# Performance work log

Hardware: AMD Instinct MI355X
Metric: run time of the kernel (lower is better)

Reference implementation:

```python
import jax, jax.numpy as jnp
import numpy as np

L, H, NH, NKV, HD, FF, V = 2, 2048, 16, 2, 128, 11008, 32000
B, S, R, LORA_SCALE = 32, 64, 16, 2.0  # lora scaling = alpha/r = 32/16
PH, TD = 1024, 512
ROPE_THETA = 1e6

def _rms(x, w, eps=1e-6):
    return x * jax.lax.rsqrt(jnp.mean(x * x, axis=-1, keepdims=True) + eps) * w

def _rot_half(x):
    h = x.shape[-1] // 2
    return jnp.concatenate([-x[..., h:], x[..., :h]], axis=-1)

def _lora_linear(x, W, A, Bm, b=None):
    y = x @ W.T + LORA_SCALE * ((x @ A.T) @ Bm.T)
    return y + b if b is not None else y

def _forward(input_ids, attention_mask, embed, Wq, bq, Aq, Bq, Wk, bk, Ak, Bk,
             Wv, bv, Av, Bv, Wo, Ao, Bo, ln1, ln2, Wg, Wu, Wd, norm_f,
             W1, b1, W2, b2):
    Bsz, Sl = input_ids.shape
    h = embed[input_ids]                                            # [B,S,H]
    inv_freq = 1.0 / (ROPE_THETA ** (jnp.arange(0, HD, 2, dtype=jnp.float32) / HD))
    ang = jnp.arange(Sl, dtype=jnp.float32)[:, None] * inv_freq      # [S,HD/2]
    cos = jnp.concatenate([jnp.cos(ang)] * 2, -1)[None, :, None, :]  # [1,S,1,HD]
    sin = jnp.concatenate([jnp.sin(ang)] * 2, -1)[None, :, None, :]
    causal = jnp.tril(jnp.ones((Sl, Sl), dtype=bool))
    keep = causal[None, None] & (attention_mask[:, None, None, :] > 0)
    bias = jnp.where(keep, 0.0, -1e9).astype(jnp.float32)            # [B,1,S,S]
    for l in range(L):
        x = _rms(h, ln1[l])
        q = _lora_linear(x, Wq[l], Aq[l], Bq[l], bq[l]).reshape(Bsz, Sl, NH, HD)
        k = _lora_linear(x, Wk[l], Ak[l], Bk[l], bk[l]).reshape(Bsz, Sl, NKV, HD)
        v = _lora_linear(x, Wv[l], Av[l], Bv[l], bv[l]).reshape(Bsz, Sl, NKV, HD)
        q = q * cos + _rot_half(q) * sin
        k = k * cos + _rot_half(k) * sin
        k = jnp.repeat(k, NH // NKV, axis=2)                         # GQA expand
        v = jnp.repeat(v, NH // NKV, axis=2)
        scores = jnp.einsum('bqhd,bkhd->bhqk', q, k) / np.sqrt(HD).astype(np.float32) + bias
        p = jax.nn.softmax(scores, axis=-1)
        attn = jnp.einsum('bhqk,bkhd->bqhd', p, v).reshape(Bsz, Sl, H)
        h = h + _lora_linear(attn, Wo[l], Ao[l], Bo[l])
        x = _rms(h, ln2[l])
        h = h + (jax.nn.silu(x @ Wg[l].T) * (x @ Wu[l].T)) @ Wd[l].T  # SwiGLU MLP
    h = _rms(h, norm_f)                       # final norm -> hidden_states[-1]
    seq_len = jnp.sum(attention_mask, axis=1) - 1
    pooled = h[jnp.arange(Bsz), seq_len]      # last valid token  [B,H]
    z = jax.nn.gelu(pooled @ W1.T + b1, approximate=False)
    return (z @ W2.T + b2).astype(jnp.float32)  # [B,512]

def setup_inputs():
    key = jax.random.key(0)
    ks = jax.random.split(key, 32)
    def n(k, shape, s=0.02):
        return (s * jax.random.normal(k, shape)).astype(jnp.float32)
    lens = jax.random.randint(ks[0], (B,), 1, S + 1)
    return {
        'input_ids': jax.random.randint(ks[1], (B, S), 0, V, dtype=jnp.int32),
        'attention_mask': (jnp.arange(S)[None, :] < lens[:, None]).astype(jnp.int32),
        'embed': n(ks[2], (V, H)),
        'Wq': n(ks[3], (L, H, H)), 'bq': n(ks[4], (L, H)),
        'Aq': n(ks[5], (L, R, H)), 'Bq': n(ks[6], (L, H, R)),
        'Wk': n(ks[7], (L, NKV * HD, H)), 'bk': n(ks[8], (L, NKV * HD)),
        'Ak': n(ks[9], (L, R, H)), 'Bk': n(ks[10], (L, NKV * HD, R)),
        'Wv': n(ks[11], (L, NKV * HD, H)), 'bv': n(ks[12], (L, NKV * HD)),
        'Av': n(ks[13], (L, R, H)), 'Bv': n(ks[14], (L, NKV * HD, R)),
        'Wo': n(ks[15], (L, H, H)),
        'Ao': n(ks[16], (L, R, H)), 'Bo': n(ks[17], (L, H, R)),
        'ln1': jnp.ones((L, H), jnp.float32), 'ln2': jnp.ones((L, H), jnp.float32),
        'Wg': n(ks[18], (L, FF, H)), 'Wu': n(ks[19], (L, FF, H)), 'Wd': n(ks[20], (L, H, FF)),
        'norm_f': jnp.ones((H,), jnp.float32),
        'W1': n(ks[21], (PH, H)), 'b1': jnp.zeros((PH,), jnp.float32),
        'W2': n(ks[22], (TD, PH)), 'b2': jnp.zeros((TD,), jnp.float32),
    }

def reference(input_ids, attention_mask, embed, Wq, bq, Aq, Bq, Wk, bk, Ak, Bk,
              Wv, bv, Av, Bv, Wo, Ao, Bo, ln1, ln2, Wg, Wu, Wd, norm_f,
              W1, b1, W2, b2):
    return _forward(input_ids, attention_mask, embed, Wq, bq, Aq, Bq, Wk, bk, Ak, Bk,
                    Wv, bv, Av, Bv, Wo, Ao, Bo, ln1, ln2, Wg, Wu, Wd, norm_f,
                    W1, b1, W2, b2)
```

## Files before the change

kernel.cpp:

```cpp
#include <hip/hip_runtime.h>
#include <hip/hip_bf16.h>
#include <math.h>

namespace {
constexpr int NL  = 2;
constexpr int H   = 2048;
constexpr int NH  = 16;
constexpr int NKV = 2;
constexpr int HD  = 128;
constexpr int FF  = 11008;
constexpr int BB  = 32;
constexpr int SS  = 64;
constexpr int RR  = 16;
constexpr int TT  = BB * SS;
constexpr int KVD = NKV * HD;
constexpr int QKVD = H + 2 * KVD;
constexpr int PH  = 1024, TDm = 512;
constexpr float LSCALE = 2.0f;
}

typedef __bf16 bf16x8 __attribute__((ext_vector_type(8)));
typedef float  f32x4  __attribute__((ext_vector_type(4)));

__device__ __forceinline__ ushort4 f4_to_bf4(float4 r) {
  __hip_bfloat16 a = __float2bfloat16(r.x), b = __float2bfloat16(r.y),
                 c = __float2bfloat16(r.z), d = __float2bfloat16(r.w);
  return make_ushort4(*(unsigned short*)&a, *(unsigned short*)&b,
                      *(unsigned short*)&c, *(unsigned short*)&d);
}

__global__ __launch_bounds__(256) void k_embed(const int* __restrict__ ids,
                                               const float* __restrict__ emb,
                                               float* __restrict__ h) {
  int t = blockIdx.x;
  long id = ids[t];
  const float4* src = reinterpret_cast<const float4*>(emb + id * (long)H);
  float4* dst = reinterpret_cast<float4*>(h + (long)t * H);
  for (int i = threadIdx.x; i < H / 4; i += 256) dst[i] = src[i];
}

__global__ __launch_bounds__(256) void k_cvt(const float* __restrict__ src,
                                             __hip_bfloat16* __restrict__ dst, long n) {
  long i = ((long)blockIdx.x * 256 + threadIdx.x) * 4;
  if (i >= n) return;
  float4 v = *reinterpret_cast<const float4*>(src + i);
  *reinterpret_cast<ushort4*>(dst + i) = f4_to_bf4(v);
}

__global__ __launch_bounds__(256) void k_rmsnorm(const float* __restrict__ in,
                                                 const float* __restrict__ w,
                                                 float* __restrict__ out,
                                                 __hip_bfloat16* __restrict__ outb) {
  int t = blockIdx.x, tid = threadIdx.x;
  const float4* xr = reinterpret_cast<const float4*>(in + (long)t * H);
  float4 v0 = xr[tid], v1 = xr[tid + 256];
  float ss = v0.x*v0.x + v0.y*v0.y + v0.z*v0.z + v0.w*v0.w
           + v1.x*v1.x + v1.y*v1.y + v1.z*v1.z + v1.w*v1.w;
  #pragma unroll
  for (int off = 32; off; off >>= 1) ss += __shfl_xor(ss, off);
  __shared__ float sred[4];
  if ((tid & 63) == 0) sred[tid >> 6] = ss;
  __syncthreads();
  float scale = rsqrtf((sred[0] + sred[1] + sred[2] + sred[3]) * (1.0f / H) + 1e-6f);
  const float4* wr = reinterpret_cast<const float4*>(w);
  float4 w0 = wr[tid], w1 = wr[tid + 256];
  float4 r0 = make_float4(v0.x*scale*w0.x, v0.y*scale*w0.y, v0.z*scale*w0.z, v0.w*scale*w0.w);
  float4 r1 = make_float4(v1.x*scale*w1.x, v1.y*scale*w1.y, v1.z*scale*w1.z, v1.w*scale*w1.w);
  float4* o = reinterpret_cast<float4*>(out + (long)t * H);
  o[tid] = r0; o[tid + 256] = r1;
  ushort4* ob = reinterpret_cast<ushort4*>(outb + (long)t * H);
  ob[tid] = f4_to_bf4(r0); ob[tid + 256] = f4_to_bf4(r1);
}

enum { ME_BIAS_F32 = 0, ME_ACC_F32 = 1, ME_SILU_BF16 = 2, ME_MUL_BF16 = 3 };

__device__ __forceinline__ int raster_sw(int bid, int nwg) {
  int q8 = nwg >> 3, r8 = nwg & 7;
  int xcd = bid & 7, pos = bid >> 3;
  return (xcd < r8 ? xcd * (q8 + 1) : r8 * (q8 + 1) + (xcd - r8) * q8) + pos;
}

template <int EPI, int BM, int BN, int WROWS, int WCOLS>
__global__ __launch_bounds__(256) void k_mgemm(
    const __hip_bfloat16* __restrict__ Abf,
    const __hip_bfloat16* __restrict__ Wbf,
    const float* __restrict__ bias,
    float* __restrict__ Cf,
    __hip_bfloat16* Cb,
    const __hip_bfloat16* gate,
    int M, int N, int K) {
  constexpr int BK = 32;
  constexpr int WTM = BM / WROWS, WTN = BN / WCOLS;
  constexpr int FM = WTM / 16, FN = WTN / 16;
  constexpr int ACH = BM * BK / 8, BCH = BN * BK / 8;
  __shared__ __align__(16) __bf16 As[2][BM * BK];
  __shared__ __align__(16) __bf16 Bs[2][BN * BK];
  const int tid = threadIdx.x;
  const int sw = raster_sw(blockIdx.x, gridDim.x);
  const int ntm = M / BM;
  const int bm = (sw % ntm) * BM, bn = (sw / ntm) * BN;
  const int lane = tid & 63, wv = tid >> 6;
  const int wm = (wv / WCOLS) * WTM, wn = (wv % WCOLS) * WTN;
  const int lr15 = lane & 15;
  const int lks = (((lane >> 4) << 3)) ^ ((((lr15 >> 1) & 3)) << 3);
  f32x4 acc[FM][FN] = {};
  const __bf16* Ag = reinterpret_cast<const __bf16*>(Abf) + (long)bm * K;
  const __bf16* Bg = reinterpret_cast<const __bf16*>(Wbf) + (long)bn * K;

  auto stage = [&](int buf, int k0) {
    #pragma unroll
    for (int i = tid; i < ACH; i += 256)
      __builtin_amdgcn_global_load_lds(
          (const __attribute__((address_space(1))) void*)
            (Ag + (long)(i >> 2) * K + k0 + (((i & 3) ^ ((i >> 3) & 3)) << 3)),
          (__attribute__((address_space(3))) void*)(&As[buf][i * 8]), 16, 0, 0);
    #pragma unroll
    for (int i = tid; i < BCH; i += 256)
      __builtin_amdgcn_global_load_lds(
          (const __attribute__((address_space(1))) void*)
            (Bg + (long)(i >> 2) * K + k0 + (((i & 3) ^ ((i >> 3) & 3)) << 3)),
          (__attribute__((address_space(3))) void*)(&Bs[buf][i * 8]), 16, 0, 0);
  };
  auto compute = [&](int buf) {
    bf16x8 af[FM], bfr[FN];
    #pragma unroll
    for (int m = 0; m < FM; ++m)
      af[m] = *reinterpret_cast<const bf16x8*>(&As[buf][(wm + m * 16 + lr15) * BK + lks]);
    #pragma unroll
    for (int n = 0; n < FN; ++n)
      bfr[n] = *reinterpret_cast<const bf16x8*>(&Bs[buf][(wn + n * 16 + lr15) * BK + lks]);
    #pragma unroll
    for (int m = 0; m < FM; ++m)
      #pragma unroll
      for (int n = 0; n < FN; ++n)
        acc[m][n] = __builtin_amdgcn_mfma_f32_16x16x32_bf16(af[m], bfr[n], acc[m][n], 0, 0, 0);
  };

  stage(0, 0);
  asm volatile("s_waitcnt vmcnt(0)" ::: "memory");
  __builtin_amdgcn_s_barrier();
  int cur = 0;
  for (int k0 = BK; k0 < K; k0 += BK) {
    stage(cur ^ 1, k0);
    compute(cur);
    asm volatile("s_waitcnt vmcnt(0)" ::: "memory");
    __builtin_amdgcn_s_barrier();
    cur ^= 1;
  }
  compute(cur);

  const int r0 = (lane >> 4) << 2;
  #pragma unroll
  for (int m = 0; m < FM; ++m)
    #pragma unroll
    for (int n = 0; n < FN; ++n) {
      const int col = bn + wn + n * 16 + lr15;
      const long rowb = bm + wm + m * 16 + r0;
      #pragma unroll
      for (int j = 0; j < 4; ++j) {
        const long off = (rowb + j) * N + col;
        float v = acc[m][n][j];
        if constexpr (EPI == ME_BIAS_F32) {
          Cf[off] = v + bias[col];
        } else if constexpr (EPI == ME_ACC_F32) {
          Cf[off] += v;
        } else if constexpr (EPI == ME_SILU_BF16) {
          Cb[off] = __float2bfloat16(v / (1.0f + expf(-v)));
        } else {
          float g = __bfloat162float(gate[off]);
          Cb[off] = __float2bfloat16(v * g);
        }
      }
    }
}

template <int BM, int BN, int WROWS, int WCOLS>
__global__ __launch_bounds__(256, 2) void k_swiglu(
    const __hip_bfloat16* __restrict__ Abf,
    const __hip_bfloat16* __restrict__ Wgb,
    const __hip_bfloat16* __restrict__ Wub,
    __hip_bfloat16* __restrict__ Cb,
    int M, int N, int K) {
  constexpr int BK = 32;
  constexpr int WTM = BM / WROWS, WTN = BN / WCOLS;
  constexpr int FM = WTM / 16, FN = WTN / 16;
  constexpr int ACH = BM * BK / 8, BCH = BN * BK / 8;
  __shared__ __align__(16) __bf16 As[2][BM * BK];
  __shared__ __align__(16) __bf16 Gs[2][BN * BK];
  __shared__ __align__(16) __bf16 Us[2][BN * BK];
  const int tid = threadIdx.x;
  const int sw = raster_sw(blockIdx.x, gridDim.x);
  const int ntm = M / BM;
  const int bm = (sw % ntm) * BM, bn = (sw / ntm) * BN;
  const int lane = tid & 63, wv = tid >> 6;
  const int wm = (wv / WCOLS) * WTM, wn = (wv % WCOLS) * WTN;
  const int lr15 = lane & 15;
  const int lks = (((lane >> 4) << 3)) ^ ((((lr15 >> 1) & 3)) << 3);
  f32x4 accg[FM][FN] = {}, accu[FM][FN] = {};
  const __bf16* Ag = reinterpret_cast<const __bf16*>(Abf) + (long)bm * K;
  const __bf16* Gg = reinterpret_cast<const __bf16*>(Wgb) + (long)bn * K;
  const __bf16* Ug = reinterpret_cast<const __bf16*>(Wub) + (long)bn * K;

  auto stage = [&](int buf, int k0) {
    #pragma unroll
    for (int i = tid; i < ACH; i += 256)
      __builtin_amdgcn_global_load_lds(
          (const __attribute__((address_space(1))) void*)
            (Ag + (long)(i >> 2) * K + k0 + (((i & 3) ^ ((i >> 3) & 3)) << 3)),
          (__attribute__((address_space(3))) void*)(&As[buf][i * 8]), 16, 0, 0);
    #pragma unroll
    for (int i = tid; i < BCH; i += 256)
      __builtin_amdgcn_global_load_lds(
          (const __attribute__((address_space(1))) void*)
            (Gg + (long)(i >> 2) * K + k0 + (((i & 3) ^ ((i >> 3) & 3)) << 3)),
          (__attribute__((address_space(3))) void*)(&Gs[buf][i * 8]), 16, 0, 0);
    #pragma unroll
    for (int i = tid; i < BCH; i += 256)
      __builtin_amdgcn_global_load_lds(
          (const __attribute__((address_space(1))) void*)
            (Ug + (long)(i >> 2) * K + k0 + (((i & 3) ^ ((i >> 3) & 3)) << 3)),
          (__attribute__((address_space(3))) void*)(&Us[buf][i * 8]), 16, 0, 0);
  };
  auto compute = [&](int buf) {
    bf16x8 af[FM], gf[FN], uf[FN];
    #pragma unroll
    for (int m = 0; m < FM; ++m)
      af[m] = *reinterpret_cast<const bf16x8*>(&As[buf][(wm + m * 16 + lr15) * BK + lks]);
    #pragma unroll
    for (int n = 0; n < FN; ++n) {
      gf[n] = *reinterpret_cast<const bf16x8*>(&Gs[buf][(wn + n * 16 + lr15) * BK + lks]);
      uf[n] = *reinterpret_cast<const bf16x8*>(&Us[buf][(wn + n * 16 + lr15) * BK + lks]);
    }
    #pragma unroll
    for (int m = 0; m < FM; ++m)
      #pragma unroll
      for (int n = 0; n < FN; ++n) {
        accg[m][n] = __builtin_amdgcn_mfma_f32_16x16x32_bf16(af[m], gf[n], accg[m][n], 0, 0, 0);
        accu[m][n] = __builtin_amdgcn_mfma_f32_16x16x32_bf16(af[m], uf[n], accu[m][n], 0, 0, 0);
      }
  };

  stage(0, 0);
  asm volatile("s_waitcnt vmcnt(0)" ::: "memory");
  __builtin_amdgcn_s_barrier();
  int cur = 0;
  for (int k0 = BK; k0 < K; k0 += BK) {
    stage(cur ^ 1, k0);
    compute(cur);
    asm volatile("s_waitcnt vmcnt(0)" ::: "memory");
    __builtin_amdgcn_s_barrier();
    cur ^= 1;
  }
  compute(cur);

  const int r0 = (lane >> 4) << 2;
  #pragma unroll
  for (int m = 0; m < FM; ++m)
    #pragma unroll
    for (int n = 0; n < FN; ++n) {
      const int col = bn + wn + n * 16 + lr15;
      const long rowb = bm + wm + m * 16 + r0;
      #pragma unroll
      for (int j = 0; j < 4; ++j) {
        float g = accg[m][n][j], u = accu[m][n][j];
        Cb[(rowb + j) * N + col] = __float2bfloat16((g / (1.0f + expf(-g))) * u);
      }
    }
}

enum { EPI_STORE = 0, EPI_GELU = 3 };

template <int EPI, bool HAS_BIAS>
__global__ __launch_bounds__(256) void k_gemm(const float* __restrict__ A,
                                              const float* __restrict__ W,
                                              const float* __restrict__ bias,
                                              float* __restrict__ C,
                                              int M, int N, int K) {
  constexpr int BM = 64, BN = 64, BK = 16;
  __shared__ float As[BK][BM + 4];
  __shared__ float Ws[BK][BN + 4];
  const int bm = blockIdx.y * BM, bn = blockIdx.x * BN;
  const int tid = threadIdx.x;
  const int lr = tid >> 2;
  const int lc = (tid & 3) << 2;
  const int ty = tid >> 4, tx = tid & 15;
  float acc[4][4] = {};
  const int arow = bm + lr;
  const bool aok = arow < M;
  const float* Ap = A + (long)arow * K + lc;
  const float* Wp = W + (long)(bn + lr) * K + lc;
  for (int k0 = 0; k0 < K; k0 += BK) {
    float4 av = aok ? *reinterpret_cast<const float4*>(Ap + k0) : make_float4(0.f, 0.f, 0.f, 0.f);
    float4 wv = *reinterpret_cast<const float4*>(Wp + k0);
    As[lc + 0][lr] = av.x; As[lc + 1][lr] = av.y; As[lc + 2][lr] = av.z; As[lc + 3][lr] = av.w;
    Ws[lc + 0][lr] = wv.x; Ws[lc + 1][lr] = wv.y; Ws[lc + 2][lr] = wv.z; Ws[lc + 3][lr] = wv.w;
    __syncthreads();
    #pragma unroll
    for (int k = 0; k < BK; ++k) {
      float4 a4 = *reinterpret_cast<const float4*>(&As[k][ty << 2]);
      float4 b4 = *reinterpret_cast<const float4*>(&Ws[k][tx << 2]);
      float a[4] = {a4.x, a4.y, a4.z, a4.w};
      float b[4] = {b4.x, b4.y, b4.z, b4.w};
      #pragma unroll
      for (int i = 0; i < 4; ++i)
        #pragma unroll
        for (int j = 0; j < 4; ++j) acc[i][j] = fmaf(a[i], b[j], acc[i][j]);
    }
    __syncthreads();
  }
  const int col = bn + (tx << 2);
  #pragma unroll
  for (int i = 0; i < 4; ++i) {
    int row = bm + (ty << 2) + i;
    if (row < M) {
      float4 r = make_float4(acc[i][0], acc[i][1], acc[i][2], acc[i][3]);
      if (HAS_BIAS) {
        float4 bv = *reinterpret_cast<const float4*>(bias + col);
        r.x += bv.x; r.y += bv.y; r.z += bv.z; r.w += bv.w;
      }
      if (EPI == EPI_GELU) {
        r.x = 0.5f * r.x * (1.0f + erff(r.x * 0.70710678118654752f));
        r.y = 0.5f * r.y * (1.0f + erff(r.y * 0.70710678118654752f));
        r.z = 0.5f * r.z * (1.0f + erff(r.z * 0.70710678118654752f));
        r.w = 0.5f * r.w * (1.0f + erff(r.w * 0.70710678118654752f));
      }
      *reinterpret_cast<float4*>(C + (long)row * N + col) = r;
    }
  }
}

__global__ __launch_bounds__(256) void k_lora_down(const float* __restrict__ x,
                                                   const float* __restrict__ A,
                                                   float* __restrict__ tmp) {
  int t = blockIdx.x, tid = threadIdx.x;
  int r = tid & 15, sl = tid >> 4;
  const float* xr = x + (long)t * H + sl * 128;
  const float* Ar = A + (long)r * H + sl * 128;
  float p = 0.f;
  #pragma unroll 8
  for (int kk = 0; kk < 128; kk += 4) {
    float4 xv = *reinterpret_cast<const float4*>(xr + kk);
    float4 av = *reinterpret_cast<const float4*>(Ar + kk);
    p = fmaf(xv.x, av.x, p); p = fmaf(xv.y, av.y, p);
    p = fmaf(xv.z, av.z, p); p = fmaf(xv.w, av.w, p);
  }
  __shared__ float red[16][17];
  red[sl][r] = p;
  __syncthreads();
  if (tid < 16) {
    float s = 0.f;
    #pragma unroll
    for (int i = 0; i < 16; ++i) s += red[i][tid];
    tmp[t * RR + tid] = s;
  }
}

__global__ __launch_bounds__(256) void k_lora_add(const float* __restrict__ tmp,
                                                  const float* __restrict__ Bm,
                                                  float* __restrict__ C, int ldC, int N) {
  long idx = (long)blockIdx.x * 256 + threadIdx.x;
  if (idx >= (long)TT * N) return;
  int t = (int)(idx / N), n = (int)(idx % N);
  const float* tr = tmp + (long)t * RR;
  const float* br = Bm + (long)n * RR;
  float s = 0.f;
  #pragma unroll
  for (int r = 0; r < RR; ++r) s = fmaf(tr[r], br[r], s);
  C[(long)t * ldC + n] += LSCALE * s;
}

__global__ __launch_bounds__(256) void k_rope(float* __restrict__ qkv) {
  int t = blockIdx.x;
  float pos = (float)(t & (SS - 1));
  float* row = qkv + (long)t * QKVD;
  for (int idx = threadIdx.x; idx < NH * 64 + NKV * 64; idx += 256) {
    float* base;
    int j;
    if (idx < NH * 64) {
      int head = idx >> 6; j = idx & 63;
      base = row + head * HD;
    } else {
      int i2 = idx - NH * 64;
      int head = i2 >> 6; j = i2 & 63;
      base = row + H + head * HD;
    }
    float inv = 1.0f / powf(1.0e6f, (float)(2 * j) * (1.0f / HD));
    float ang = pos * inv;
    float cs = cosf(ang), sn = sinf(ang);
    float lo = base[j], hi = base[j + 64];
    base[j]      = lo * cs - hi * sn;
    base[j + 64] = hi * cs + lo * sn;
  }
}

__global__ __launch_bounds__(64) void k_attn(const float* __restrict__ qkv,
                                             const int* __restrict__ mask,
                                             float* __restrict__ o,
                                             __hip_bfloat16* __restrict__ obf) {
  int flat = blockIdx.x;
  int qi = flat & (SS - 1);
  int hh = (flat >> 6) & (NH - 1);
  int b  = flat >> 10;
  int lane = threadIdx.x;
  int kv = hh >> 3;
  long t = (long)b * SS + qi;
  const float* qr = qkv + t * QKVD + hh * HD;
  const float* kr = qkv + ((long)b * SS + lane) * QKVD + H + kv * HD;
  float dot = 0.f;
  #pragma unroll 8
  for (int d = 0; d < HD; d += 4) {
    float4 qv = *reinterpret_cast<const float4*>(qr + d);
    float4 kvv = *reinterpret_cast<const float4*>(kr + d);
    dot = fmaf(qv.x, kvv.x, dot); dot = fmaf(qv.y, kvv.y, dot);
    dot = fmaf(qv.z, kvv.z, dot); dot = fmaf(qv.w, kvv.w, dot);
  }
  bool keep = (lane <= qi) && (mask[b * SS + lane] > 0);
  float sc = dot * 0.08838834764831845f + (keep ? 0.f : -1e9f);
  float m = sc;
  #pragma unroll
  for (int off = 32; off; off >>= 1) m = fmaxf(m, __shfl_xor(m, off));
  float e = expf(sc - m);
  float s = e;
  #pragma unroll
  for (int off = 32; off; off >>= 1) s += __shfl_xor(s, off);
  float p = e / s;
  __shared__ float pl[64];
  pl[lane] = p;
  __syncthreads();
  float o0 = 0.f, o1 = 0.f;
  const float* vb = qkv + (long)b * SS * QKVD + H + KVD + kv * HD;
  for (int ki = 0; ki < SS; ++ki) {
    float pp = pl[ki];
    o0 = fmaf(pp, vb[(long)ki * QKVD + lane], o0);
    o1 = fmaf(pp, vb[(long)ki * QKVD + lane + 64], o1);
  }
  long oidx = t * H + hh * HD + lane;
  o[oidx] = o0;
  o[oidx + 64] = o1;
  __hip_bfloat16 b0 = __float2bfloat16(o0), b1 = __float2bfloat16(o1);
  obf[oidx] = b0;
  obf[oidx + 64] = b1;
}

__global__ __launch_bounds__(256) void k_pool(const float* __restrict__ x,
                                              const int* __restrict__ mask,
                                              float* __restrict__ pooled) {
  int b = blockIdx.x;
  __shared__ int len;
  if (threadIdx.x == 0) {
    int L2 = 0;
    for (int i = 0; i < SS; ++i) L2 += (mask[b * SS + i] > 0);
    len = L2;
  }
  __syncthreads();
  const float4* sp = reinterpret_cast<const float4*>(x + ((long)b * SS + len - 1) * H);
  float4* dp = reinterpret_cast<float4*>(pooled + (long)b * H);
  for (int i = threadIdx.x; i < H / 4; i += 256) dp[i] = sp[i];
}

static inline int cvt_grid(long n) { return (int)((n / 4 + 255) / 256); }

extern "C" void kernel_launch(void* const* d_in, const int* in_sizes, int n_in,
                              void* d_out, int out_size, void* d_ws, size_t ws_size,
                              hipStream_t stream) {
  const int*   ids    = (const int*)d_in[0];
  const int*   mask   = (const int*)d_in[1];
  const float* embed  = (const float*)d_in[2];
  const float* Wq     = (const float*)d_in[3];
  const float* bq     = (const float*)d_in[4];
  const float* Aq     = (const float*)d_in[5];
  const float* Bq     = (const float*)d_in[6];
  const float* Wk     = (const float*)d_in[7];
  const float* bk     = (const float*)d_in[8];
  const float* Ak     = (const float*)d_in[9];
  const float* Bk     = (const float*)d_in[10];
  const float* Wv     = (const float*)d_in[11];
  const float* bv     = (const float*)d_in[12];
  const float* Av     = (const float*)d_in[13];
  const float* Bv     = (const float*)d_in[14];
  const float* Wo     = (const float*)d_in[15];
  const float* Ao     = (const float*)d_in[16];
  const float* Bo     = (const float*)d_in[17];
  const float* ln1    = (const float*)d_in[18];
  const float* ln2    = (const float*)d_in[19];
  const float* Wg     = (const float*)d_in[20];
  const float* Wu     = (const float*)d_in[21];
  const float* Wd     = (const float*)d_in[22];
  const float* norm_f = (const float*)d_in[23];
  const float* W1     = (const float*)d_in[24];
  const float* b1     = (const float*)d_in[25];
  const float* W2     = (const float*)d_in[26];
  const float* b2     = (const float*)d_in[27];

  float* ws = (float*)d_ws;
  float* h       = ws;
  float* x       = h    + (long)TT * H;
  float* qkv     = x    + (long)TT * H;
  float* tmpR    = qkv  + (long)TT * QKVD;
  float* pooled  = tmpR + (long)TT * RR;
  float* zz      = pooled + (long)BB * H;
  float* biascat = zz   + (long)BB * PH;
  float* endf32  = biascat + QKVD;
  __hip_bfloat16* x_bf = (__hip_bfloat16*)endf32;
  __hip_bfloat16* ffbf = x_bf + (long)TT * H;
  __hip_bfloat16* wbf  = ffbf + (long)TT * FF;
  __hip_bfloat16* wbf2 = wbf  + (long)FF * H;
  size_t need_fused = (size_t)((char*)(wbf2 + (long)FF * H) - (char*)d_ws);
  bool fused_ok = ws_size >= need_fused;

  k_embed<<<TT, 256, 0, stream>>>(ids, embed, h);

  for (int l = 0; l < NL; ++l) {
    const long lHH = (long)l * H * H;
    const long lKH = (long)l * KVD * H;
    const long lRH = (long)l * RR * H;
    k_rmsnorm<<<TT, 256, 0, stream>>>(h, ln1 + l * H, x, x_bf);
    k_cvt<<<cvt_grid((long)H * H), 256, 0, stream>>>(Wq + lHH, wbf, (long)H * H);
    k_cvt<<<cvt_grid((long)KVD * H), 256, 0, stream>>>(Wk + lKH, wbf + (long)H * H, (long)KVD * H);
    k_cvt<<<cvt_grid((long)KVD * H), 256, 0, stream>>>(Wv + lKH, wbf + (long)(H + KVD) * H, (long)KVD * H);
    hipMemcpyAsync(biascat,           bq + (long)l * H,   H * sizeof(float),   hipMemcpyDeviceToDevice, stream);
    hipMemcpyAsync(biascat + H,       bk + (long)l * KVD, KVD * sizeof(float), hipMemcpyDeviceToDevice, stream);
    hipMemcpyAsync(biascat + H + KVD, bv + (long)l * KVD, KVD * sizeof(float), hipMemcpyDeviceToDevice, stream);
    k_mgemm<ME_BIAS_F32, 128, 128, 2, 2><<<(TT / 128) * (QKVD / 128), 256, 0, stream>>>(
        x_bf, wbf, biascat, qkv, nullptr, nullptr, TT, QKVD, H);
    k_lora_down<<<TT, 256, 0, stream>>>(x, Aq + lRH, tmpR);
    k_lora_add<<<((long)TT * H + 255) / 256, 256, 0, stream>>>(tmpR, Bq + (long)l * H * RR, qkv, QKVD, H);
    k_lora_down<<<TT, 256, 0, stream>>>(x, Ak + lRH, tmpR);
    k_lora_add<<<((long)TT * KVD + 255) / 256, 256, 0, stream>>>(tmpR, Bk + (long)l * KVD * RR, qkv + H, QKVD, KVD);
    k_lora_down<<<TT, 256, 0, stream>>>(x, Av + lRH, tmpR);
    k_lora_add<<<((long)TT * KVD + 255) / 256, 256, 0, stream>>>(tmpR, Bv + (long)l * KVD * RR, qkv + H + KVD, QKVD, KVD);
    k_rope<<<TT, 256, 0, stream>>>(qkv);
    k_attn<<<BB * NH * SS, 64, 0, stream>>>(qkv, mask, x, x_bf);
    k_lora_down<<<TT, 256, 0, stream>>>(x, Ao + lRH, tmpR);
    k_cvt<<<cvt_grid((long)H * H), 256, 0, stream>>>(Wo + lHH, wbf, (long)H * H);
    k_mgemm<ME_ACC_F32, 64, 128, 2, 2><<<(TT / 64) * (H / 128), 256, 0, stream>>>(
        x_bf, wbf, nullptr, h, nullptr, nullptr, TT, H, H);
    k_lora_add<<<((long)TT * H + 255) / 256, 256, 0, stream>>>(tmpR, Bo + (long)l * H * RR, h, H, H);
    k_rmsnorm<<<TT, 256, 0, stream>>>(h, ln2 + l * H, x, x_bf);
    if (fused_ok) {
      k_cvt<<<cvt_grid((long)FF * H), 256, 0, stream>>>(Wg + (long)l * FF * H, wbf, (long)FF * H);
      k_cvt<<<cvt_grid((long)FF * H), 256, 0, stream>>>(Wu + (long)l * FF * H, wbf2, (long)FF * H);
      k_swiglu<128, 128, 2, 2><<<(TT / 128) * (FF / 128), 256, 0, stream>>>(
          x_bf, wbf, wbf2, ffbf, TT, FF, H);
    } else {
      k_cvt<<<cvt_grid((long)FF * H), 256, 0, stream>>>(Wg + (long)l * FF * H, wbf, (long)FF * H);
      k_mgemm<ME_SILU_BF16, 128, 128, 2, 2><<<(TT / 128) * (FF / 128), 256, 0, stream>>>(
          x_bf, wbf, nullptr, nullptr, ffbf, nullptr, TT, FF, H);
      k_cvt<<<cvt_grid((long)FF * H), 256, 0, stream>>>(Wu + (long)l * FF * H, wbf, (long)FF * H);
      k_mgemm<ME_MUL_BF16, 128, 128, 2, 2><<<(TT / 128) * (FF / 128), 256, 0, stream>>>(
          x_bf, wbf, nullptr, nullptr, ffbf, ffbf, TT, FF, H);
    }
    k_cvt<<<cvt_grid((long)H * FF), 256, 0, stream>>>(Wd + (long)l * H * FF, wbf, (long)H * FF);
    k_mgemm<ME_ACC_F32, 64, 128, 2, 2><<<(TT / 64) * (H / 128), 256, 0, stream>>>(
        ffbf, wbf, nullptr, h, nullptr, nullptr, TT, H, FF);
  }

  k_rmsnorm<<<TT, 256, 0, stream>>>(h, norm_f, x, x_bf);
  k_pool<<<BB, 256, 0, stream>>>(x, mask, pooled);
  k_gemm<EPI_GELU, true><<<dim3(PH / 64, 1), 256, 0, stream>>>(pooled, W1, b1, zz, BB, PH, H);
  k_gemm<EPI_STORE, true><<<dim3(TDm / 64, 1), 256, 0, stream>>>(zz, W2, b2, (float*)d_out, BB, TDm, PH);
}
```

Measured before the change: 2.146 ms.

## Triple-buffer GEMM LDS staging with partial vmcnt waits; enlarge Wo/Wd tiles

The MFMA GEMM and fused SwiGLU kernels go from double to triple buffering. Two k-slabs are prefetched ahead, and a partial s_waitcnt vmcnt waits only for the oldest stage's loads, so global-to-LDS loads overlap more compute. The Wo and Wd projection GEMMs also switch from 64x128 to 128x128 tiles, raising reuse but halving the grid to 256 blocks. Triple buffering raises LDS use per block, which may lower occupancy, especially for the SwiGLU kernel with three operand buffers.

```diff
diff --git a/kernel.cpp b/kernel.cpp
--- a/kernel.cpp
+++ b/kernel.cpp
@@ -29,6 +29,16 @@
                       *(unsigned short*)&c, *(unsigned short*)&d);
 }
 
+template <int N> __device__ __forceinline__ void wait_vm() {
+  static_assert(N == 0 || N == 3 || N == 4 || N == 6 || N == 8 || N == 12, "add case");
+  if constexpr (N == 0)      asm volatile("s_waitcnt vmcnt(0)" ::: "memory");
+  else if constexpr (N == 3) asm volatile("s_waitcnt vmcnt(3)" ::: "memory");
+  else if constexpr (N == 4) asm volatile("s_waitcnt vmcnt(4)" ::: "memory");
+  else if constexpr (N == 6) asm volatile("s_waitcnt vmcnt(6)" ::: "memory");
+  else if constexpr (N == 8) asm volatile("s_waitcnt vmcnt(8)" ::: "memory");
+  else                       asm volatile("s_waitcnt vmcnt(12)" ::: "memory");
+}
+
 __global__ __launch_bounds__(256) void k_embed(const int* __restrict__ ids,
                                                const float* __restrict__ emb,
                                                float* __restrict__ h) {
@@ -93,8 +103,9 @@
   constexpr int WTM = BM / WROWS, WTN = BN / WCOLS;
   constexpr int FM = WTM / 16, FN = WTN / 16;
   constexpr int ACH = BM * BK / 8, BCH = BN * BK / 8;
-  __shared__ __align__(16) __bf16 As[2][BM * BK];
-  __shared__ __align__(16) __bf16 Bs[2][BN * BK];
+  constexpr int LPT = (ACH + BCH) / 256;
+  __shared__ __align__(16) __bf16 As[3][BM * BK];
+  __shared__ __align__(16) __bf16 Bs[3][BN * BK];
   const int tid = threadIdx.x;
   const int sw = raster_sw(blockIdx.x, gridDim.x);
   const int ntm = M / BM;
@@ -136,18 +147,20 @@
         acc[m][n] = __builtin_amdgcn_mfma_f32_16x16x32_bf16(af[m], bfr[n], acc[m][n], 0, 0, 0);
   };
 
+  const int NS = K / BK;
   stage(0, 0);
-  asm volatile("s_waitcnt vmcnt(0)" ::: "memory");
+  stage(1, BK);
+  wait_vm<LPT>();
   __builtin_amdgcn_s_barrier();
-  int cur = 0;
-  for (int k0 = BK; k0 < K; k0 += BK) {
-    stage(cur ^ 1, k0);
-    compute(cur);
-    asm volatile("s_waitcnt vmcnt(0)" ::: "memory");
-    __builtin_amdgcn_s_barrier();
-    cur ^= 1;
-  }
-  compute(cur);
+  for (int t = 0; t < NS; ++t) {
+    if (t + 2 < NS) stage((t + 2) % 3, (t + 2) * BK);
+    compute(t % 3);
+    if (t + 1 < NS) {
+      if (t + 2 < NS) wait_vm<LPT>();
+      else            wait_vm<0>();
+      __builtin_amdgcn_s_barrier();
+    }
+  }
 
   const int r0 = (lane >> 4) << 2;
   #pragma unroll
@@ -185,9 +198,10 @@
   constexpr int WTM = BM / WROWS, WTN = BN / WCOLS;
   constexpr int FM = WTM / 16, FN = WTN / 16;
   constexpr int ACH = BM * BK / 8, BCH = BN * BK / 8;
-  __shared__ __align__(16) __bf16 As[2][BM * BK];
-  __shared__ __align__(16) __bf16 Gs[2][BN * BK];
-  __shared__ __align__(16) __bf16 Us[2][BN * BK];
+  constexpr int LPT = (ACH + 2 * BCH) / 256;
+  __shared__ __align__(16) __bf16 As[3][BM * BK];
+  __shared__ __align__(16) __bf16 Gs[3][BN * BK];
+  __shared__ __align__(16) __bf16 Us[3][BN * BK];
   const int tid = threadIdx.x;
   const int sw = raster_sw(blockIdx.x, gridDim.x);
   const int ntm = M / BM;
@@ -240,18 +254,20 @@
       }
   };
 
+  const int NS = K / BK;
   stage(0, 0);
-  asm volatile("s_waitcnt vmcnt(0)" ::: "memory");
+  stage(1, BK);
+  wait_vm<LPT>();
   __builtin_amdgcn_s_barrier();
-  int cur = 0;
-  for (int k0 = BK; k0 < K; k0 += BK) {
-    stage(cur ^ 1, k0);
-    compute(cur);
-    asm volatile("s_waitcnt vmcnt(0)" ::: "memory");
-    __builtin_amdgcn_s_barrier();
-    cur ^= 1;
-  }
-  compute(cur);
+  for (int t = 0; t < NS; ++t) {
+    if (t + 2 < NS) stage((t + 2) % 3, (t + 2) * BK);
+    compute(t % 3);
+    if (t + 1 < NS) {
+      if (t + 2 < NS) wait_vm<LPT>();
+      else            wait_vm<0>();
+      __builtin_amdgcn_s_barrier();
+    }
+  }
 
   const int r0 = (lane >> 4) << 2;
   #pragma unroll
@@ -533,7 +549,7 @@
     k_attn<<<BB * NH * SS, 64, 0, stream>>>(qkv, mask, x, x_bf);
     k_lora_down<<<TT, 256, 0, stream>>>(x, Ao + lRH, tmpR);
     k_cvt<<<cvt_grid((long)H * H), 256, 0, stream>>>(Wo + lHH, wbf, (long)H * H);
-    k_mgemm<ME_ACC_F32, 64, 128, 2, 2><<<(TT / 64) * (H / 128), 256, 0, stream>>>(
+    k_mgemm<ME_ACC_F32, 128, 128, 2, 2><<<(TT / 128) * (H / 128), 256, 0, stream>>>(
         x_bf, wbf, nullptr, h, nullptr, nullptr, TT, H, H);
     k_lora_add<<<((long)TT * H + 255) / 256, 256, 0, stream>>>(tmpR, Bo + (long)l * H * RR, h, H, H);
     k_rmsnorm<<<TT, 256, 0, stream>>>(h, ln2 + l * H, x, x_bf);
@@ -551,7 +567,7 @@
           x_bf, wbf, nullptr, nullptr, ffbf, ffbf, TT, FF, H);
     }
     k_cvt<<<cvt_grid((long)H * FF), 256, 0, stream>>>(Wd + (long)l * H * FF, wbf, (long)H * FF);
-    k_mgemm<ME_ACC_F32, 64, 128, 2, 2><<<(TT / 64) * (H / 128), 256, 0, stream>>>(
+    k_mgemm<ME_ACC_F32, 128, 128, 2, 2><<<(TT / 128) * (H / 128), 256, 0, stream>>>(
         ffbf, wbf, nullptr, h, nullptr, nullptr, TT, H, FF);
   }
 
```

New measurement: 2.353 ms. +9.6%, slower.

## Use 512-thread 128x128 GEMM tiles and precompute RoPE cos/sin table

Applied to the files above, without the earlier changes.

Fixes the mfma GEMM kernel at 128x128 tiles with 8 waves (2x4 warp grid, 64x32 per wave) and 512 threads, including the Wo and down projections that previously used 64x128 tiles. This halves the block count for those two GEMMs and doubles the waves per block, aiming for more reuse per tile and better latency hiding. RoPE cos/sin values are now computed once into a workspace table instead of calling powf/cosf/sinf per element in every layer. Larger tiles on the N=2048 GEMMs leave only 256 blocks, which may underfill the GPU.

```diff
diff --git a/kernel.cpp b/kernel.cpp
--- a/kernel.cpp
+++ b/kernel.cpp
@@ -80,8 +80,8 @@
   return (xcd < r8 ? xcd * (q8 + 1) : r8 * (q8 + 1) + (xcd - r8) * q8) + pos;
 }
 
-template <int EPI, int BM, int BN, int WROWS, int WCOLS>
-__global__ __launch_bounds__(256) void k_mgemm(
+template <int EPI>
+__global__ __launch_bounds__(512) void k_mgemm(
     const __hip_bfloat16* __restrict__ Abf,
     const __hip_bfloat16* __restrict__ Wbf,
     const float* __restrict__ bias,
@@ -89,9 +89,8 @@
     __hip_bfloat16* Cb,
     const __hip_bfloat16* gate,
     int M, int N, int K) {
-  constexpr int BK = 32;
-  constexpr int WTM = BM / WROWS, WTN = BN / WCOLS;
-  constexpr int FM = WTM / 16, FN = WTN / 16;
+  constexpr int BM = 128, BN = 128, BK = 32;
+  constexpr int FM = 4, FN = 2;
   constexpr int ACH = BM * BK / 8, BCH = BN * BK / 8;
   __shared__ __align__(16) __bf16 As[2][BM * BK];
   __shared__ __align__(16) __bf16 Bs[2][BN * BK];
@@ -100,7 +99,7 @@
   const int ntm = M / BM;
   const int bm = (sw % ntm) * BM, bn = (sw / ntm) * BN;
   const int lane = tid & 63, wv = tid >> 6;
-  const int wm = (wv / WCOLS) * WTM, wn = (wv % WCOLS) * WTN;
+  const int wm = (wv >> 2) * 64, wn = (wv & 3) * 32;
   const int lr15 = lane & 15;
   const int lks = (((lane >> 4) << 3)) ^ ((((lr15 >> 1) & 3)) << 3);
   f32x4 acc[FM][FN] = {};
@@ -109,13 +108,13 @@
 
   auto stage = [&](int buf, int k0) {
     #pragma unroll
-    for (int i = tid; i < ACH; i += 256)
+    for (int i = tid; i < ACH; i += 512)
       __builtin_amdgcn_global_load_lds(
           (const __attribute__((address_space(1))) void*)
             (Ag + (long)(i >> 2) * K + k0 + (((i & 3) ^ ((i >> 3) & 3)) << 3)),
           (__attribute__((address_space(3))) void*)(&As[buf][i * 8]), 16, 0, 0);
     #pragma unroll
-    for (int i = tid; i < BCH; i += 256)
+    for (int i = tid; i < BCH; i += 512)
       __builtin_amdgcn_global_load_lds(
           (const __attribute__((address_space(1))) void*)
             (Bg + (long)(i >> 2) * K + k0 + (((i & 3) ^ ((i >> 3) & 3)) << 3)),
@@ -369,9 +368,19 @@
   C[(long)t * ldC + n] += LSCALE * s;
 }
 
-__global__ __launch_bounds__(256) void k_rope(float* __restrict__ qkv) {
+__global__ __launch_bounds__(256) void k_rope_tab(float2* __restrict__ tab) {
+  int idx = blockIdx.x * 256 + threadIdx.x;
+  if (idx >= SS * 64) return;
+  int pos = idx >> 6, j = idx & 63;
+  float inv = 1.0f / powf(1.0e6f, (float)(2 * j) * (1.0f / HD));
+  float ang = (float)pos * inv;
+  tab[idx] = make_float2(cosf(ang), sinf(ang));
+}
+
+__global__ __launch_bounds__(256) void k_rope(float* __restrict__ qkv,
+                                              const float2* __restrict__ tab) {
   int t = blockIdx.x;
-  float pos = (float)(t & (SS - 1));
+  const float2* trow = tab + (t & (SS - 1)) * 64;
   float* row = qkv + (long)t * QKVD;
   for (int idx = threadIdx.x; idx < NH * 64 + NKV * 64; idx += 256) {
     float* base;
@@ -384,12 +393,10 @@
       int head = i2 >> 6; j = i2 & 63;
       base = row + H + head * HD;
     }
-    float inv = 1.0f / powf(1.0e6f, (float)(2 * j) * (1.0f / HD));
-    float ang = pos * inv;
-    float cs = cosf(ang), sn = sinf(ang);
+    float2 cs2 = trow[j];
     float lo = base[j], hi = base[j + 64];
-    base[j]      = lo * cs - hi * sn;
-    base[j + 64] = hi * cs + lo * sn;
+    base[j]      = lo * cs2.x - hi * cs2.y;
+    base[j + 64] = hi * cs2.x + lo * cs2.y;
   }
 }
 
@@ -500,7 +507,8 @@
   float* pooled  = tmpR + (long)TT * RR;
   float* zz      = pooled + (long)BB * H;
   float* biascat = zz   + (long)BB * PH;
-  float* endf32  = biascat + QKVD;
+  float2* ropetab = (float2*)(biascat + QKVD);
+  float* endf32  = (float*)(ropetab + SS * 64);
   __hip_bfloat16* x_bf = (__hip_bfloat16*)endf32;
   __hip_bfloat16* ffbf = x_bf + (long)TT * H;
   __hip_bfloat16* wbf  = ffbf + (long)TT * FF;
@@ -509,6 +517,7 @@
   bool fused_ok = ws_size >= need_fused;
 
   k_embed<<<TT, 256, 0, stream>>>(ids, embed, h);
+  k_rope_tab<<<(SS * 64 + 255) / 256, 256, 0, stream>>>(ropetab);
 
   for (int l = 0; l < NL; ++l) {
     const long lHH = (long)l * H * H;
@@ -521,7 +530,7 @@
     hipMemcpyAsync(biascat,           bq + (long)l * H,   H * sizeof(float),   hipMemcpyDeviceToDevice, stream);
     hipMemcpyAsync(biascat + H,       bk + (long)l * KVD, KVD * sizeof(float), hipMemcpyDeviceToDevice, stream);
     hipMemcpyAsync(biascat + H + KVD, bv + (long)l * KVD, KVD * sizeof(float), hipMemcpyDeviceToDevice, stream);
-    k_mgemm<ME_BIAS_F32, 128, 128, 2, 2><<<(TT / 128) * (QKVD / 128), 256, 0, stream>>>(
+    k_mgemm<ME_BIAS_F32><<<(TT / 128) * (QKVD / 128), 512, 0, stream>>>(
         x_bf, wbf, biascat, qkv, nullptr, nullptr, TT, QKVD, H);
     k_lora_down<<<TT, 256, 0, stream>>>(x, Aq + lRH, tmpR);
     k_lora_add<<<((long)TT * H + 255) / 256, 256, 0, stream>>>(tmpR, Bq + (long)l * H * RR, qkv, QKVD, H);
@@ -529,11 +538,11 @@
     k_lora_add<<<((long)TT * KVD + 255) / 256, 256, 0, stream>>>(tmpR, Bk + (long)l * KVD * RR, qkv + H, QKVD, KVD);
     k_lora_down<<<TT, 256, 0, stream>>>(x, Av + lRH, tmpR);
     k_lora_add<<<((long)TT * KVD + 255) / 256, 256, 0, stream>>>(tmpR, Bv + (long)l * KVD * RR, qkv + H + KVD, QKVD, KVD);
-    k_rope<<<TT, 256, 0, stream>>>(qkv);
+    k_rope<<<TT, 256, 0, stream>>>(qkv, ropetab);
     k_attn<<<BB * NH * SS, 64, 0, stream>>>(qkv, mask, x, x_bf);
     k_lora_down<<<TT, 256, 0, stream>>>(x, Ao + lRH, tmpR);
     k_cvt<<<cvt_grid((long)H * H), 256, 0, stream>>>(Wo + lHH, wbf, (long)H * H);
-    k_mgemm<ME_ACC_F32, 64, 128, 2, 2><<<(TT / 64) * (H / 128), 256, 0, stream>>>(
+    k_mgemm<ME_ACC_F32><<<(TT / 128) * (H / 128), 512, 0, stream>>>(
         x_bf, wbf, nullptr, h, nullptr, nullptr, TT, H, H);
     k_lora_add<<<((long)TT * H + 255) / 256, 256, 0, stream>>>(tmpR, Bo + (long)l * H * RR, h, H, H);
     k_rmsnorm<<<TT, 256, 0, stream>>>(h, ln2 + l * H, x, x_bf);
@@ -544,14 +553,14 @@
           x_bf, wbf, wbf2, ffbf, TT, FF, H);
     } else {
       k_cvt<<<cvt_grid((long)FF * H), 256, 0, stream>>>(Wg + (long)l * FF * H, wbf, (long)FF * H);
-      k_mgemm<ME_SILU_BF16, 128, 128, 2, 2><<<(TT / 128) * (FF / 128), 256, 0, stream>>>(
+      k_mgemm<ME_SILU_BF16><<<(TT / 128) * (FF / 128), 512, 0, stream>>>(
           x_bf, wbf, nullptr, nullptr, ffbf, nullptr, TT, FF, H);
       k_cvt<<<cvt_grid((long)FF * H), 256, 0, stream>>>(Wu + (long)l * FF * H, wbf, (long)FF * H);
-      k_mgemm<ME_MUL_BF16, 128, 128, 2, 2><<<(TT / 128) * (FF / 128), 256, 0, stream>>>(
+      k_mgemm<ME_MUL_BF16><<<(TT / 128) * (FF / 128), 512, 0, stream>>>(
           x_bf, wbf, nullptr, nullptr, ffbf, ffbf, TT, FF, H);
     }
     k_cvt<<<cvt_grid((long)H * FF), 256, 0, stream>>>(Wd + (long)l * H * FF, wbf, (long)H * FF);
-    k_mgemm<ME_ACC_F32, 64, 128, 2, 2><<<(TT / 64) * (H / 128), 256, 0, stream>>>(
+    k_mgemm<ME_ACC_F32><<<(TT / 128) * (H / 128), 512, 0, stream>>>(
         ffbf, wbf, nullptr, h, nullptr, nullptr, TT, H, FF);
   }
 
```

Result: no change. 2.117 ms (-1.4%).
